# Kernel tuning notes

Measured on AMD Instinct MI355X. Metric: run time of the kernel, lower is better.

## Reference

```python
import jax, jax.numpy as jnp
import numpy as np

UNITS = 512

def _c(r, i):
    return jax.lax.complex(r, i)

# BSSD's elementwise_* activations act on real and imag parts separately (split activation)
def _csig(z):
    return _c(jax.nn.sigmoid(z.real), jax.nn.sigmoid(z.imag))

def _ctanh(z):
    return _c(jnp.tanh(z.real), jnp.tanh(z.imag))

def setup_inputs() -> dict:
    key = jax.random.key(0)
    ks = jax.random.split(key, 6)
    B, T, N, U = 16, 2000, 512, UNITS
    f = lambda k, s, sc: jax.random.normal(k, s, jnp.float32) * sc
    return {
        'x_real': f(ks[0], (B, T, N), 1.0),
        'x_imag': f(ks[1], (B, T, N), 1.0),
        'W_real': f(ks[2], (N, 4 * U), 0.03),
        'W_imag': f(ks[3], (N, 4 * U), 0.03),
        'U_real': f(ks[4], (U, 4 * U), 0.03),
        'U_imag': f(ks[5], (U, 4 * U), 0.03),
        'b_real': jnp.zeros((4 * U,), jnp.float32),
        'b_imag': jnp.zeros((4 * U,), jnp.float32),
    }

def reference(x_real, x_imag, W_real, W_imag, U_real, U_imag, b_real, b_imag):
    Uc = UNITS
    x = _c(x_real, x_imag)                       # [B,T,N] complex64
    W = _c(W_real, W_imag)                       # [N,4U]
    Um = _c(U_real, U_imag)                      # [U,4U]
    b = _c(b_real, b_imag)                       # [4U]
    # input contribution precomputed for all steps (one big GEMM)
    zx = jnp.einsum('bti,ij->btj', x, W) + b     # [B,T,4U]
    zx = jnp.swapaxes(zx, 0, 1)                  # [T,B,4U]
    B = x.shape[0]
    h0 = jnp.zeros((B, Uc), zx.dtype)
    c0 = jnp.zeros((B, Uc), zx.dtype)

    def step(carry, z_t):
        h, c = carry
        z = z_t + h @ Um                         # [B,4U]
        a = _ctanh(z[:, :Uc])
        i = _csig(z[:, Uc:2 * Uc])
        f = _csig(z[:, 2 * Uc:3 * Uc])
        o = _csig(z[:, 3 * Uc:])
        c = a * i + f * c
        h = o * _ctanh(c)                        # activation='tanh'
        return (h, c), h

    _, hs = jax.lax.scan(step, (h0, c0), zx)     # [T,B,U]
    hs = jnp.swapaxes(hs, 0, 1)                  # [B,T,U]
    # return real/imag stacked so output dtype is float32
    return jnp.stack([hs.real, hs.imag], axis=-1)  # [B,T,U,2]
```

## Files before the change

### kernel.cpp

```cpp
#include <hip/hip_runtime.h>
#include <cstdint>
#include <cstddef>

#define B_   16
#define T_   2000
#define NIN  512
#define U_   512
#define G4   2048
#define KP   1024
#define JP   4096
#define M_   32000
#define NGRP 8
#define MPG  32
#define SCAN_BLOCKS (NGRP * MPG)
#define LDSROW 2112

typedef __attribute__((ext_vector_type(8))) short bf16x8;
typedef __attribute__((ext_vector_type(4))) float f32x4;
typedef __attribute__((ext_vector_type(2))) int i32x2;

#define MFMA(a, b, c) __builtin_amdgcn_mfma_f32_16x16x32_bf16((a), (b), (c), 0, 0, 0)

__device__ __forceinline__ unsigned short f2bf(float f) {
  unsigned u = __builtin_bit_cast(unsigned, f);
  u = (u + 0x7FFFu + ((u >> 16) & 1u)) >> 16;
  return (unsigned short)u;
}
__device__ __forceinline__ float bf2f(unsigned short h) {
  unsigned u = ((unsigned)h) << 16;
  return __builtin_bit_cast(float, u);
}
__device__ __forceinline__ float sigm(float x) {
  return 1.0f / (1.0f + __expf(-x));
}
__device__ __forceinline__ float tanh_f(float x) {
  float cx = fminf(fmaxf(x, -15.0f), 15.0f);
  float e = __expf(2.0f * cx);
  return (e - 1.0f) / (e + 1.0f);
}

__device__ __forceinline__ void ld32_l3_sync(const void* p, uint4& a, uint4& b) {
  asm volatile("global_load_dwordx4 %0, %2, off sc0 sc1\n\t"
               "global_load_dwordx4 %1, %3, off sc0 sc1\n\t"
               "s_waitcnt vmcnt(0)"
               : "=&v"(a), "=&v"(b)
               : "v"(p), "v"((const void*)((const char*)p + 16))
               : "memory");
  __builtin_amdgcn_sched_barrier(0);
}
__device__ __forceinline__ void st8_l3(void* p, i32x2 v) {
  asm volatile("global_store_dwordx2 %0, %1, off sc0 sc1" :: "v"(p), "v"(v) : "memory");
}

__global__ __launch_bounds__(256) void k_convert_x(const float* __restrict__ xr,
                                                   const float* __restrict__ xi,
                                                   unsigned short* __restrict__ Ab) {
  int i = blockIdx.x * 256 + threadIdx.x;
  int m = i >> 6;
  int k0 = (i & 63) << 3;
  if (m >= M_) return;
  const float* pr = xr + (size_t)m * NIN + k0;
  const float* pi = xi + (size_t)m * NIN + k0;
  float4 r0 = *reinterpret_cast<const float4*>(pr);
  float4 r1 = *reinterpret_cast<const float4*>(pr + 4);
  float4 i0 = *reinterpret_cast<const float4*>(pi);
  float4 i1 = *reinterpret_cast<const float4*>(pi + 4);
  uint4 v0, v1;
  v0.x = f2bf(r0.x) | ((unsigned)f2bf(i0.x) << 16);
  v0.y = f2bf(r0.y) | ((unsigned)f2bf(i0.y) << 16);
  v0.z = f2bf(r0.z) | ((unsigned)f2bf(i0.z) << 16);
  v0.w = f2bf(r0.w) | ((unsigned)f2bf(i0.w) << 16);
  v1.x = f2bf(r1.x) | ((unsigned)f2bf(i1.x) << 16);
  v1.y = f2bf(r1.y) | ((unsigned)f2bf(i1.y) << 16);
  v1.z = f2bf(r1.z) | ((unsigned)f2bf(i1.z) << 16);
  v1.w = f2bf(r1.w) | ((unsigned)f2bf(i1.w) << 16);
  unsigned short* dst = Ab + (size_t)m * KP + 2 * k0;
  *reinterpret_cast<uint4*>(dst) = v0;
  *reinterpret_cast<uint4*>(dst + 8) = v1;
}

__global__ __launch_bounds__(256) void k_pack_B(const float* __restrict__ Wr,
                                                const float* __restrict__ Wi,
                                                unsigned short* __restrict__ Bt) {
  int i = blockIdx.x * 256 + threadIdx.x;
  if (i >= JP * KP) return;
  int jp = i >> 10;
  int k = i & 1023;
  int p = jp >> 11;
  int j = jp & 2047;
  int u = k >> 1;
  int pl = k & 1;
  float v;
  if (p == 0) {
    v = pl ? -Wi[(size_t)u * G4 + j] : Wr[(size_t)u * G4 + j];
  } else {
    v = pl ? Wr[(size_t)u * G4 + j] : Wi[(size_t)u * G4 + j];
  }
  Bt[i] = f2bf(v);
}

__global__ __launch_bounds__(256) void k_gemm_zx(const unsigned short* __restrict__ A,
                                                 const unsigned short* __restrict__ Bt,
                                                 unsigned short* __restrict__ zx) {
  int bid = blockIdx.x;
  int nt = bid & 31;
  int mt = bid >> 5;
  int tid = threadIdx.x;
  int lane = tid & 63;
  int wid = tid >> 6;
  int wm = wid >> 1, wn = wid & 1;
  int l15 = lane & 15;
  int kb = (lane >> 4) << 3;
  int rowb = mt * 128 + wm * 64;
  int colb = nt * 128 + wn * 64;

  const unsigned short* ap[4];
  const unsigned short* bp[4];
#pragma unroll
  for (int x = 0; x < 4; ++x) {
    ap[x] = A + (size_t)(rowb + x * 16 + l15) * KP + kb;
    bp[x] = Bt + (size_t)(colb + x * 16 + l15) * KP + kb;
  }

  f32x4 acc[4][4];
#pragma unroll
  for (int mi = 0; mi < 4; ++mi)
#pragma unroll
    for (int ni = 0; ni < 4; ++ni) acc[mi][ni] = (f32x4){0.f, 0.f, 0.f, 0.f};

#pragma unroll 2
  for (int k = 0; k < KP; k += 32) {
    bf16x8 av[4], bv[4];
#pragma unroll
    for (int x = 0; x < 4; ++x) {
      av[x] = *reinterpret_cast<const bf16x8*>(ap[x] + k);
      bv[x] = *reinterpret_cast<const bf16x8*>(bp[x] + k);
    }
#pragma unroll
    for (int mi = 0; mi < 4; ++mi)
#pragma unroll
      for (int ni = 0; ni < 4; ++ni)
        acc[mi][ni] = MFMA(av[mi], bv[ni], acc[mi][ni]);
  }

  int rq = (lane >> 4) << 2;
#pragma unroll
  for (int mi = 0; mi < 4; ++mi) {
#pragma unroll
    for (int r = 0; r < 4; ++r) {
      int m = rowb + mi * 16 + rq + r;
      int bbv = m / T_;
      int tv = m - bbv * T_;
      size_t rowoff = (size_t)(tv * 16 + bbv) * (G4 * 2);
#pragma unroll
      for (int ni = 0; ni < 4; ++ni) {
        int jp2 = colb + ni * 16 + l15;
        int p = jp2 >> 11;
        int j = jp2 & 2047;
        zx[rowoff + (size_t)j * 2 + p] = f2bf(acc[mi][ni][r]);
      }
    }
  }
}

__global__ __launch_bounds__(512, 2) void k_scan(
    const unsigned short* __restrict__ zx,
    const unsigned short* __restrict__ Ub,
    const float* __restrict__ brp,
    const float* __restrict__ bip,
    char* __restrict__ hb2,
    float* __restrict__ out) {
  const int bid = blockIdx.x;
  const int tid = threadIdx.x;
  const int lane = tid & 63;
  const int w = tid >> 6;
  const int l15 = lane & 15;
  const int g = bid & 7;
  const int m = bid >> 3;

  __shared__ char lds_h[2 * LDSROW];
  __shared__ float zp[2][132];

  const int p_ = w >> 2, q_ = w & 3;
  const unsigned short* uptr =
      Ub + (size_t)(p_ * 2048 + q_ * 512 + m * 16 + l15) * KP + ((lane >> 4) << 3);
  bf16x8 uf[32];
#pragma unroll
  for (int kk = 0; kk < 32; ++kk)
    uf[kk] = *reinterpret_cast<const bf16x8*>(uptr + kk * 32);
#pragma unroll
  for (int kk = 0; kk < 32; ++kk)
    asm volatile("" : "+v"(uf[kk]));

  const int gb = tid >> 4;
  const int gu = tid & 15;
  const int u = m * 16 + gu;
  const int bglob = g * 2 + gb;
  float brg[4], big[4];
  if (tid < 32) {
#pragma unroll
    for (int q = 0; q < 4; ++q) {
      brg[q] = brp[q * 512 + u];
      big[q] = bip[q * 512 + u];
    }
  }
  float cr = 0.f, ci = 0.f;

  char* hgrp = hb2 + (size_t)g * 16384;

  const int srow = tid >> 7;
  const int sbyte = (tid & 127) * 16;

  const int arow = (l15 & 1) * LDSROW;
  const int achunk = (lane >> 4) * 16;

  unsigned zprev[4];
  if (tid < 32) {
    const unsigned* zt = (const unsigned*)zx + (size_t)bglob * 2048;
#pragma unroll
    for (int q = 0; q < 4; ++q) zprev[q] = zt[q * 512 + u];
  }

  for (int t = 0; t < T_; ++t) {
    const int par = t & 1;

    if (tid < 256) {
      const char* src = hgrp + par * 8192 + tid * 32;
      uint4 v0, v1;
      for (;;) {
        ld32_l3_sync(src, v0, v1);
        if ((int)v0.y >= t && (int)v0.w >= t &&
            (int)v1.y >= t && (int)v1.w >= t) break;
        __builtin_amdgcn_s_sleep(1);
      }
      uint4 hq;
      hq.x = v0.x;
      hq.y = v0.z;
      hq.z = v1.x;
      hq.w = v1.z;
      *reinterpret_cast<uint4*>(lds_h + srow * LDSROW + sbyte) = hq;
    }
    __syncthreads();

    unsigned zloc[4];
    if (tid < 32) {
#pragma unroll
      for (int q = 0; q < 4; ++q) zloc[q] = zprev[q];
      int tp = t + 1 < T_ ? t + 1 : t;
      const unsigned* zt = (const unsigned*)zx + (size_t)(tp * 16 + bglob) * 2048;
#pragma unroll
      for (int q = 0; q < 4; ++q) zprev[q] = zt[q * 512 + u];
    }

    f32x4 a0 = {0.f, 0.f, 0.f, 0.f};
    f32x4 a1 = {0.f, 0.f, 0.f, 0.f};
    f32x4 a2 = {0.f, 0.f, 0.f, 0.f};
    f32x4 a3 = {0.f, 0.f, 0.f, 0.f};
#pragma unroll
    for (int kk = 0; kk < 32; kk += 4) {
      bf16x8 x0 = *reinterpret_cast<const bf16x8*>(lds_h + arow + (kk + 0) * 64 + achunk);
      bf16x8 x1 = *reinterpret_cast<const bf16x8*>(lds_h + arow + (kk + 1) * 64 + achunk);
      bf16x8 x2 = *reinterpret_cast<const bf16x8*>(lds_h + arow + (kk + 2) * 64 + achunk);
      bf16x8 x3 = *reinterpret_cast<const bf16x8*>(lds_h + arow + (kk + 3) * 64 + achunk);
      a0 = MFMA(x0, uf[kk + 0], a0);
      a1 = MFMA(x1, uf[kk + 1], a1);
      a2 = MFMA(x2, uf[kk + 2], a2);
      a3 = MFMA(x3, uf[kk + 3], a3);
    }
    if (lane < 16) {
      f32x4 s = (a0 + a1) + (a2 + a3);
      zp[0][w * 16 + lane] = s[0];
      zp[1][w * 16 + lane] = s[1];
    }
    __syncthreads();

    if (tid < 32) {
      float zr[4], zi[4];
#pragma unroll
      for (int q = 0; q < 4; ++q) {
        zr[q] = zp[gb][q * 16 + gu] + brg[q] +
                bf2f((unsigned short)(zloc[q] & 0xFFFFu));
        zi[q] = zp[gb][64 + q * 16 + gu] + big[q] +
                bf2f((unsigned short)(zloc[q] >> 16));
      }
      float ar = tanh_f(zr[0]), ai = tanh_f(zi[0]);
      float ir = sigm(zr[1]), ii = sigm(zi[1]);
      float fr = sigm(zr[2]), fi = sigm(zi[2]);
      float og_r = sigm(zr[3]), og_i = sigm(zi[3]);
      float ncr = ar * ir - ai * ii + fr * cr - fi * ci;
      float nci = ar * ii + ai * ir + fr * ci + fi * cr;
      cr = ncr;
      ci = nci;
      float tr = tanh_f(cr), ti = tanh_f(ci);
      float hr = og_r * tr - og_i * ti;
      float hi = og_r * ti + og_i * tr;

      i32x2 rec;
      rec.x = (int)((unsigned)f2bf(hr) | ((unsigned)f2bf(hi) << 16));
      rec.y = t + 1;
      st8_l3(hgrp + (par ^ 1) * 8192 + (size_t)(gb * 512 + u) * 8, rec);

      float2 hv;
      hv.x = hr;
      hv.y = hi;
      *reinterpret_cast<float2*>(out + ((size_t)(bglob * T_ + t) * U_ + u) * 2) = hv;
    }
  }
}

extern "C" void kernel_launch(void* const* d_in, const int* in_sizes, int n_in,
                              void* d_out, int out_size, void* d_ws, size_t ws_size,
                              hipStream_t stream) {
  const float* xr = (const float*)d_in[0];
  const float* xi = (const float*)d_in[1];
  const float* Wr = (const float*)d_in[2];
  const float* Wi = (const float*)d_in[3];
  const float* Ur = (const float*)d_in[4];
  const float* Ui = (const float*)d_in[5];
  const float* br = (const float*)d_in[6];
  const float* bi = (const float*)d_in[7];

  const size_t SZ_ZX = (size_t)M_ * G4 * 2 * 2;
  const size_t SZ_AB = (size_t)M_ * KP * 2;
  const size_t SZ_BT = (size_t)JP * KP * 2;
  const size_t SZ_HB2 = (size_t)NGRP * 16384;
  const size_t OFF_ZX = 0;
  const size_t OFF_AB = OFF_ZX + SZ_ZX;
  const size_t OFF_BW = OFF_AB + SZ_AB;
  const size_t OFF_BU = OFF_BW + SZ_BT;
  const size_t OFF_HB = OFF_BU + SZ_BT;
  const size_t NEEDED = OFF_HB + SZ_HB2;
  if (ws_size < NEEDED) return;

  char* ws = (char*)d_ws;
  unsigned short* zx = (unsigned short*)(ws + OFF_ZX);
  unsigned short* Ab = (unsigned short*)(ws + OFF_AB);
  unsigned short* BtW = (unsigned short*)(ws + OFF_BW);
  unsigned short* BtU = (unsigned short*)(ws + OFF_BU);
  char* hb2 = ws + OFF_HB;

  hipMemsetAsync(ws + OFF_HB, 0, SZ_HB2, stream);

  hipLaunchKernelGGL(k_convert_x, dim3(8000), dim3(256), 0, stream, xr, xi, Ab);
  hipLaunchKernelGGL(k_pack_B, dim3(16384), dim3(256), 0, stream, Wr, Wi, BtW);
  hipLaunchKernelGGL(k_pack_B, dim3(16384), dim3(256), 0, stream, Ur, Ui, BtU);
  hipLaunchKernelGGL(k_gemm_zx, dim3(250 * 32), dim3(256), 0, stream, Ab, BtW, zx);
  hipLaunchKernelGGL(k_scan, dim3(SCAN_BLOCKS), dim3(512), 0, stream, zx, BtU,
                     br, bi, hb2, (float*)d_out);
}
```

Baseline: 5.416 ms.

## Split scan into two independent batch streams interleaved per step with shuffle reduction

The recurrent scan now treats the two batch rows of each group as separate streams with their own h buffers and flags. It alternates phases so one stream's MFMA work overlaps the other stream's cross-block wait. The MFMA output layout is remapped so each wave owns two units, which lets a wave shuffle replace the LDS partial-sum buffer and the second __syncthreads. The cost is twice as many global flag polls and barriers per time step, and the launch bound drops to one block per SIMD.

```diff
diff --git a/kernel.cpp b/kernel.cpp
--- a/kernel.cpp
+++ b/kernel.cpp
@@ -13,7 +13,6 @@
 #define NGRP 8
 #define MPG  32
 #define SCAN_BLOCKS (NGRP * MPG)
-#define LDSROW 2112
 
 typedef __attribute__((ext_vector_type(8))) short bf16x8;
 typedef __attribute__((ext_vector_type(4))) float f32x4;
@@ -39,13 +38,10 @@
   return (e - 1.0f) / (e + 1.0f);
 }
 
-__device__ __forceinline__ void ld32_l3_sync(const void* p, uint4& a, uint4& b) {
-  asm volatile("global_load_dwordx4 %0, %2, off sc0 sc1\n\t"
-               "global_load_dwordx4 %1, %3, off sc0 sc1\n\t"
+__device__ __forceinline__ void ld16_l3_sync(const void* p, uint4& a) {
+  asm volatile("global_load_dwordx4 %0, %1, off sc0 sc1\n\t"
                "s_waitcnt vmcnt(0)"
-               : "=&v"(a), "=&v"(b)
-               : "v"(p), "v"((const void*)((const char*)p + 16))
-               : "memory");
+               : "=&v"(a) : "v"(p) : "memory");
   __builtin_amdgcn_sched_barrier(0);
 }
 __device__ __forceinline__ void st8_l3(void* p, i32x2 v) {
@@ -163,7 +159,7 @@
   }
 }
 
-__global__ __launch_bounds__(512, 2) void k_scan(
+__global__ __launch_bounds__(512, 1) void k_scan(
     const unsigned short* __restrict__ zx,
     const unsigned short* __restrict__ Ub,
     const float* __restrict__ brp,
@@ -178,12 +174,13 @@
   const int g = bid & 7;
   const int m = bid >> 3;
 
-  __shared__ char lds_h[2 * LDSROW];
-  __shared__ float zp[2][132];
-
-  const int p_ = w >> 2, q_ = w & 3;
+  __shared__ char lds_h[2][2][2048];
+
+  const int c_ = l15 >> 1, ul_ = l15 & 1;
+  const int p_ = c_ >> 2, q_ = c_ & 3;
   const unsigned short* uptr =
-      Ub + (size_t)(p_ * 2048 + q_ * 512 + m * 16 + l15) * KP + ((lane >> 4) << 3);
+      Ub + (size_t)(p_ * 2048 + q_ * 512 + m * 16 + w * 2 + ul_) * KP +
+      ((lane >> 4) << 3);
   bf16x8 uf[32];
 #pragma unroll
   for (int kk = 0; kk < 32; ++kk)
@@ -192,120 +189,106 @@
   for (int kk = 0; kk < 32; ++kk)
     asm volatile("" : "+v"(uf[kk]));
 
-  const int gb = tid >> 4;
-  const int gu = tid & 15;
-  const int u = m * 16 + gu;
-  const int bglob = g * 2 + gb;
+  const int u = m * 16 + w * 2 + (lane & 1);
   float brg[4], big[4];
-  if (tid < 32) {
+  unsigned zvA[4], zvB[4];
+  if (lane < 2) {
 #pragma unroll
     for (int q = 0; q < 4; ++q) {
       brg[q] = brp[q * 512 + u];
       big[q] = bip[q * 512 + u];
     }
-  }
-  float cr = 0.f, ci = 0.f;
-
-  char* hgrp = hb2 + (size_t)g * 16384;
-
-  const int srow = tid >> 7;
-  const int sbyte = (tid & 127) * 16;
-
-  const int arow = (l15 & 1) * LDSROW;
+    const unsigned* zt0 = (const unsigned*)zx + (size_t)(g * 2 + 0) * 2048;
+    const unsigned* zt1 = (const unsigned*)zx + (size_t)(g * 2 + 1) * 2048;
+#pragma unroll
+    for (int q = 0; q < 4; ++q) {
+      zvA[q] = zt0[q * 512 + u];
+      zvB[q] = zt1[q * 512 + u];
+    }
+  }
+  float crA = 0.f, ciA = 0.f, crB = 0.f, ciB = 0.f;
+
+  char* hgrp = hb2 + (size_t)g * 32768;
   const int achunk = (lane >> 4) * 16;
 
-  unsigned zprev[4];
-  if (tid < 32) {
-    const unsigned* zt = (const unsigned*)zx + (size_t)bglob * 2048;
-#pragma unroll
-    for (int q = 0; q < 4; ++q) zprev[q] = zt[q * 512 + u];
-  }
-
-  for (int t = 0; t < T_; ++t) {
-    const int par = t & 1;
-
-    if (tid < 256) {
-      const char* src = hgrp + par * 8192 + tid * 32;
-      uint4 v0, v1;
-      for (;;) {
-        ld32_l3_sync(src, v0, v1);
-        if ((int)v0.y >= t && (int)v0.w >= t &&
-            (int)v1.y >= t && (int)v1.w >= t) break;
-        __builtin_amdgcn_s_sleep(1);
-      }
-      uint4 hq;
-      hq.x = v0.x;
-      hq.y = v0.z;
-      hq.z = v1.x;
-      hq.w = v1.z;
-      *reinterpret_cast<uint4*>(lds_h + srow * LDSROW + sbyte) = hq;
-    }
-    __syncthreads();
-
-    unsigned zloc[4];
-    if (tid < 32) {
-#pragma unroll
-      for (int q = 0; q < 4; ++q) zloc[q] = zprev[q];
-      int tp = t + 1 < T_ ? t + 1 : t;
-      const unsigned* zt = (const unsigned*)zx + (size_t)(tp * 16 + bglob) * 2048;
-#pragma unroll
-      for (int q = 0; q < 4; ++q) zprev[q] = zt[q * 512 + u];
-    }
-
-    f32x4 a0 = {0.f, 0.f, 0.f, 0.f};
-    f32x4 a1 = {0.f, 0.f, 0.f, 0.f};
-    f32x4 a2 = {0.f, 0.f, 0.f, 0.f};
-    f32x4 a3 = {0.f, 0.f, 0.f, 0.f};
-#pragma unroll
-    for (int kk = 0; kk < 32; kk += 4) {
-      bf16x8 x0 = *reinterpret_cast<const bf16x8*>(lds_h + arow + (kk + 0) * 64 + achunk);
-      bf16x8 x1 = *reinterpret_cast<const bf16x8*>(lds_h + arow + (kk + 1) * 64 + achunk);
-      bf16x8 x2 = *reinterpret_cast<const bf16x8*>(lds_h + arow + (kk + 2) * 64 + achunk);
-      bf16x8 x3 = *reinterpret_cast<const bf16x8*>(lds_h + arow + (kk + 3) * 64 + achunk);
-      a0 = MFMA(x0, uf[kk + 0], a0);
-      a1 = MFMA(x1, uf[kk + 1], a1);
-      a2 = MFMA(x2, uf[kk + 2], a2);
-      a3 = MFMA(x3, uf[kk + 3], a3);
-    }
-    if (lane < 16) {
-      f32x4 s = (a0 + a1) + (a2 + a3);
-      zp[0][w * 16 + lane] = s[0];
-      zp[1][w * 16 + lane] = s[1];
-    }
-    __syncthreads();
-
-    if (tid < 32) {
-      float zr[4], zi[4];
-#pragma unroll
-      for (int q = 0; q < 4; ++q) {
-        zr[q] = zp[gb][q * 16 + gu] + brg[q] +
-                bf2f((unsigned short)(zloc[q] & 0xFFFFu));
-        zi[q] = zp[gb][64 + q * 16 + gu] + big[q] +
-                bf2f((unsigned short)(zloc[q] >> 16));
-      }
-      float ar = tanh_f(zr[0]), ai = tanh_f(zi[0]);
-      float ir = sigm(zr[1]), ii = sigm(zi[1]);
-      float fr = sigm(zr[2]), fi = sigm(zi[2]);
-      float og_r = sigm(zr[3]), og_i = sigm(zi[3]);
-      float ncr = ar * ir - ai * ii + fr * cr - fi * ci;
-      float nci = ar * ii + ai * ir + fr * ci + fi * cr;
-      cr = ncr;
-      ci = nci;
-      float tr = tanh_f(cr), ti = tanh_f(ci);
-      float hr = og_r * tr - og_i * ti;
-      float hi = og_r * ti + og_i * tr;
-
-      i32x2 rec;
-      rec.x = (int)((unsigned)f2bf(hr) | ((unsigned)f2bf(hi) << 16));
-      rec.y = t + 1;
-      st8_l3(hgrp + (par ^ 1) * 8192 + (size_t)(gb * 512 + u) * 8, rec);
-
-      float2 hv;
-      hv.x = hr;
-      hv.y = hi;
-      *reinterpret_cast<float2*>(out + ((size_t)(bglob * T_ + t) * U_ + u) * 2) = hv;
-    }
-  }
+#define PHASE(S, TCUR, PAR, CR, CI, ZV)                                        \
+  {                                                                            \
+    if (tid < 256) {                                                           \
+      const char* psrc = hgrp + (S)*8192 + (PAR)*4096 + tid * 16;              \
+      uint4 pv;                                                                \
+      for (;;) {                                                               \
+        ld16_l3_sync(psrc, pv);                                                \
+        if ((int)pv.y >= (TCUR) && (int)pv.w >= (TCUR)) break;                 \
+        __builtin_amdgcn_s_sleep(1);                                           \
+      }                                                                        \
+      unsigned* ld2 = (unsigned*)(lds_h[S][PAR] + tid * 8);                    \
+      ld2[0] = pv.x;                                                           \
+      ld2[1] = pv.z;                                                           \
+    }                                                                          \
+    __syncthreads();                                                           \
+    f32x4 a0 = {0.f, 0.f, 0.f, 0.f};                                           \
+    f32x4 a1 = {0.f, 0.f, 0.f, 0.f};                                           \
+    f32x4 a2 = {0.f, 0.f, 0.f, 0.f};                                           \
+    f32x4 a3 = {0.f, 0.f, 0.f, 0.f};                                           \
+    _Pragma("unroll")                                                          \
+    for (int kk = 0; kk < 32; kk += 4) {                                       \
+      const char* ab = lds_h[S][PAR] + achunk;                                 \
+      bf16x8 x0 = *(const bf16x8*)(ab + (kk + 0) * 64);                        \
+      bf16x8 x1 = *(const bf16x8*)(ab + (kk + 1) * 64);                        \
+      bf16x8 x2 = *(const bf16x8*)(ab + (kk + 2) * 64);                        \
+      bf16x8 x3 = *(const bf16x8*)(ab + (kk + 3) * 64);                        \
+      a0 = MFMA(x0, uf[kk + 0], a0);                                           \
+      a1 = MFMA(x1, uf[kk + 1], a1);                                           \
+      a2 = MFMA(x2, uf[kk + 2], a2);                                           \
+      a3 = MFMA(x3, uf[kk + 3], a3);                                           \
+    }                                                                          \
+    float zsum = (a0[0] + a1[0]) + (a2[0] + a3[0]);                            \
+    float val[8];                                                              \
+    _Pragma("unroll")                                                          \
+    for (int cc = 0; cc < 8; ++cc)                                             \
+      val[cc] = __shfl(zsum, cc * 2 + (lane & 1));                             \
+    if (lane < 2) {                                                            \
+      float zr[4], zi[4];                                                      \
+      _Pragma("unroll")                                                        \
+      for (int q = 0; q < 4; ++q) {                                            \
+        zr[q] = val[q] + brg[q] + bf2f((unsigned short)((ZV)[q] & 0xFFFFu));   \
+        zi[q] = val[4 + q] + big[q] + bf2f((unsigned short)((ZV)[q] >> 16));   \
+      }                                                                        \
+      float ar = tanh_f(zr[0]), ai = tanh_f(zi[0]);                            \
+      float ir = sigm(zr[1]), ii = sigm(zi[1]);                                \
+      float fr = sigm(zr[2]), fi = sigm(zi[2]);                                \
+      float og_r = sigm(zr[3]), og_i = sigm(zi[3]);                            \
+      float ncr = ar * ir - ai * ii + fr * (CR) - fi * (CI);                   \
+      float nci = ar * ii + ai * ir + fr * (CI) + fi * (CR);                   \
+      (CR) = ncr;                                                              \
+      (CI) = nci;                                                              \
+      float tr = tanh_f(CR), ti = tanh_f(CI);                                  \
+      float hr = og_r * tr - og_i * ti;                                        \
+      float hi = og_r * ti + og_i * tr;                                        \
+      i32x2 rec;                                                               \
+      rec.x = (int)((unsigned)f2bf(hr) | ((unsigned)f2bf(hi) << 16));          \
+      rec.y = (TCUR) + 1;                                                      \
+      st8_l3(hgrp + (S)*8192 + ((PAR) ^ 1) * 4096 + u * 8, rec);               \
+      float2 hv;                                                               \
+      hv.x = hr;                                                               \
+      hv.y = hi;                                                               \
+      *reinterpret_cast<float2*>(                                              \
+          out + ((size_t)((g * 2 + (S)) * T_ + (TCUR)) * U_ + u) * 2) = hv;    \
+      int tp = (TCUR) + 1 < T_ ? (TCUR) + 1 : (TCUR);                          \
+      const unsigned* zt =                                                     \
+          (const unsigned*)zx + (size_t)(tp * 16 + g * 2 + (S)) * 2048;        \
+      _Pragma("unroll")                                                        \
+      for (int q = 0; q < 4; ++q) (ZV)[q] = zt[q * 512 + u];                   \
+    }                                                                          \
+  }
+
+  for (int tt = 0; tt < T_; tt += 2) {
+    PHASE(0, tt, 0, crA, ciA, zvA)
+    PHASE(1, tt, 0, crB, ciB, zvB)
+    PHASE(0, tt + 1, 1, crA, ciA, zvA)
+    PHASE(1, tt + 1, 1, crB, ciB, zvB)
+  }
+#undef PHASE
 }
 
 extern "C" void kernel_launch(void* const* d_in, const int* in_sizes, int n_in,
@@ -323,7 +306,7 @@
   const size_t SZ_ZX = (size_t)M_ * G4 * 2 * 2;
   const size_t SZ_AB = (size_t)M_ * KP * 2;
   const size_t SZ_BT = (size_t)JP * KP * 2;
-  const size_t SZ_HB2 = (size_t)NGRP * 16384;
+  const size_t SZ_HB2 = (size_t)NGRP * 32768;
   const size_t OFF_ZX = 0;
   const size_t OFF_AB = OFF_ZX + SZ_ZX;
   const size_t OFF_BW = OFF_AB + SZ_AB;
```

Measured after the change: 6.981 ms. 28.9% more time.

## Halve scan block to 256 threads, each wave holding two U column tiles

Applied to the files above, without the earlier changes.

The recurrent scan kernel drops from 512 to 256 threads per block. Each wave now keeps two 16-column tiles of the recurrent weight matrix in registers (64 bf16x8 fragments) and reuses each loaded h fragment for two MFMAs, which cuts LDS reads and block-wide barrier cost per timestep. The s_sleep in the spin-wait poll is also removed to lower wake-up latency. The cost is much higher register pressure per thread, a longer serial MFMA chain per wave, and heavier polling traffic on the global flags.

```diff
diff --git a/kernel.cpp b/kernel.cpp
--- a/kernel.cpp
+++ b/kernel.cpp
@@ -163,7 +163,7 @@
   }
 }
 
-__global__ __launch_bounds__(512, 2) void k_scan(
+__global__ __launch_bounds__(256, 1) void k_scan(
     const unsigned short* __restrict__ zx,
     const unsigned short* __restrict__ Ub,
     const float* __restrict__ brp,
@@ -181,16 +181,26 @@
   __shared__ char lds_h[2 * LDSROW];
   __shared__ float zp[2][132];
 
-  const int p_ = w >> 2, q_ = w & 3;
-  const unsigned short* uptr =
-      Ub + (size_t)(p_ * 2048 + q_ * 512 + m * 16 + l15) * KP + ((lane >> 4) << 3);
-  bf16x8 uf[32];
-#pragma unroll
-  for (int kk = 0; kk < 32; ++kk)
-    uf[kk] = *reinterpret_cast<const bf16x8*>(uptr + kk * 32);
-#pragma unroll
-  for (int kk = 0; kk < 32; ++kk)
-    asm volatile("" : "+v"(uf[kk]));
+  bf16x8 uf0[32], uf1[32];
+  {
+    const int c0 = w * 2, c1 = w * 2 + 1;
+    const unsigned short* up0 =
+        Ub + (size_t)((c0 >> 2) * 2048 + (c0 & 3) * 512 + m * 16 + l15) * KP +
+        ((lane >> 4) << 3);
+    const unsigned short* up1 =
+        Ub + (size_t)((c1 >> 2) * 2048 + (c1 & 3) * 512 + m * 16 + l15) * KP +
+        ((lane >> 4) << 3);
+#pragma unroll
+    for (int kk = 0; kk < 32; ++kk) {
+      uf0[kk] = *reinterpret_cast<const bf16x8*>(up0 + kk * 32);
+      uf1[kk] = *reinterpret_cast<const bf16x8*>(up1 + kk * 32);
+    }
+#pragma unroll
+    for (int kk = 0; kk < 32; ++kk) {
+      asm volatile("" : "+v"(uf0[kk]));
+      asm volatile("" : "+v"(uf1[kk]));
+    }
+  }
 
   const int gb = tid >> 4;
   const int gu = tid & 15;
@@ -224,14 +234,13 @@
   for (int t = 0; t < T_; ++t) {
     const int par = t & 1;
 
-    if (tid < 256) {
+    {
       const char* src = hgrp + par * 8192 + tid * 32;
       uint4 v0, v1;
       for (;;) {
         ld32_l3_sync(src, v0, v1);
         if ((int)v0.y >= t && (int)v0.w >= t &&
             (int)v1.y >= t && (int)v1.w >= t) break;
-        __builtin_amdgcn_s_sleep(1);
       }
       uint4 hq;
       hq.x = v0.x;
@@ -257,20 +266,21 @@
     f32x4 a2 = {0.f, 0.f, 0.f, 0.f};
     f32x4 a3 = {0.f, 0.f, 0.f, 0.f};
 #pragma unroll
-    for (int kk = 0; kk < 32; kk += 4) {
+    for (int kk = 0; kk < 32; kk += 2) {
       bf16x8 x0 = *reinterpret_cast<const bf16x8*>(lds_h + arow + (kk + 0) * 64 + achunk);
       bf16x8 x1 = *reinterpret_cast<const bf16x8*>(lds_h + arow + (kk + 1) * 64 + achunk);
-      bf16x8 x2 = *reinterpret_cast<const bf16x8*>(lds_h + arow + (kk + 2) * 64 + achunk);
-      bf16x8 x3 = *reinterpret_cast<const bf16x8*>(lds_h + arow + (kk + 3) * 64 + achunk);
-      a0 = MFMA(x0, uf[kk + 0], a0);
-      a1 = MFMA(x1, uf[kk + 1], a1);
-      a2 = MFMA(x2, uf[kk + 2], a2);
-      a3 = MFMA(x3, uf[kk + 3], a3);
+      a0 = MFMA(x0, uf0[kk + 0], a0);
+      a2 = MFMA(x0, uf1[kk + 0], a2);
+      a1 = MFMA(x1, uf0[kk + 1], a1);
+      a3 = MFMA(x1, uf1[kk + 1], a3);
     }
     if (lane < 16) {
-      f32x4 s = (a0 + a1) + (a2 + a3);
-      zp[0][w * 16 + lane] = s[0];
-      zp[1][w * 16 + lane] = s[1];
+      f32x4 s0 = a0 + a1;
+      f32x4 s1 = a2 + a3;
+      zp[0][(w * 2 + 0) * 16 + lane] = s0[0];
+      zp[1][(w * 2 + 0) * 16 + lane] = s0[1];
+      zp[0][(w * 2 + 1) * 16 + lane] = s1[0];
+      zp[1][(w * 2 + 1) * 16 + lane] = s1[1];
     }
     __syncthreads();
 
@@ -345,6 +355,6 @@
   hipLaunchKernelGGL(k_pack_B, dim3(16384), dim3(256), 0, stream, Wr, Wi, BtW);
   hipLaunchKernelGGL(k_pack_B, dim3(16384), dim3(256), 0, stream, Ur, Ui, BtU);
   hipLaunchKernelGGL(k_gemm_zx, dim3(250 * 32), dim3(256), 0, stream, Ab, BtW, zx);
-  hipLaunchKernelGGL(k_scan, dim3(SCAN_BLOCKS), dim3(512), 0, stream, zx, BtU,
+  hipLaunchKernelGGL(k_scan, dim3(SCAN_BLOCKS), dim3(256), 0, stream, zx, BtU,
                      br, bi, hb2, (float*)d_out);
 }
```

Result: slower. 6.954 ms (+28.4%).

## Stage zx GEMM tiles through swizzled LDS with double-buffered direct global-to-LDS loads

Applied to the files above, without the earlier changes.

The input-projection GEMM used to read A and B fragments straight from global memory into registers. Each wave duplicated those loads, and nothing overlapped them with compute. It now stages 128x64 tiles of A and Bt into double-buffered LDS using global_load_lds, XOR-swizzling columns to avoid bank conflicts, and overlaps the next tile's load with the MFMAs on the current one. This adds LDS traffic and a barrier per k-tile. It only affects the precompute GEMM, while the serial scan likely dominates total time.

```diff
diff --git a/kernel.cpp b/kernel.cpp
--- a/kernel.cpp
+++ b/kernel.cpp
@@ -14,10 +14,14 @@
 #define MPG  32
 #define SCAN_BLOCKS (NGRP * MPG)
 #define LDSROW 2112
+#define BKE  64
 
 typedef __attribute__((ext_vector_type(8))) short bf16x8;
 typedef __attribute__((ext_vector_type(4))) float f32x4;
 typedef __attribute__((ext_vector_type(2))) int i32x2;
+
+typedef __attribute__((address_space(1))) const unsigned AS1U;
+typedef __attribute__((address_space(3))) unsigned AS3U;
 
 #define MFMA(a, b, c) __builtin_amdgcn_mfma_f32_16x16x32_bf16((a), (b), (c), 0, 0, 0)
 
@@ -102,47 +106,88 @@
 __global__ __launch_bounds__(256) void k_gemm_zx(const unsigned short* __restrict__ A,
                                                  const unsigned short* __restrict__ Bt,
                                                  unsigned short* __restrict__ zx) {
+  __shared__ char AbL[2][128 * BKE * 2];
+  __shared__ char BbL[2][128 * BKE * 2];
+
   int bid = blockIdx.x;
   int nt = bid & 31;
   int mt = bid >> 5;
   int tid = threadIdx.x;
   int lane = tid & 63;
-  int wid = tid >> 6;
-  int wm = wid >> 1, wn = wid & 1;
+  int wv = tid >> 6;
+  int wm = wv >> 1, wn = wv & 1;
   int l15 = lane & 15;
-  int kb = (lane >> 4) << 3;
+  int kq = lane >> 4;
+
+  const int srow_l = lane >> 3;
+  const int scol = lane & 7;
+
+#define STAGE(BUF, KT)                                                         \
+  {                                                                            \
+    const int k0_ = (KT)*BKE;                                                  \
+    _Pragma("unroll")                                                          \
+    for (int inst = 0; inst < 4; ++inst) {                                     \
+      int r0_ = wv * 32 + inst * 8;                                            \
+      int ra_ = r0_ + srow_l;                                                  \
+      int ca_ = scol ^ (ra_ & 7);                                              \
+      const unsigned short* ga_ =                                              \
+          A + (size_t)(mt * 128 + ra_) * KP + k0_ + ca_ * 8;                   \
+      __builtin_amdgcn_global_load_lds((AS1U*)ga_,                             \
+                                       (AS3U*)&AbL[BUF][r0_ * 128], 16, 0, 0); \
+      const unsigned short* gb_ =                                              \
+          Bt + (size_t)(nt * 128 + ra_) * KP + k0_ + ca_ * 8;                  \
+      __builtin_amdgcn_global_load_lds((AS1U*)gb_,                             \
+                                       (AS3U*)&BbL[BUF][r0_ * 128], 16, 0, 0); \
+    }                                                                          \
+  }
+
+  f32x4 acc[4][4];
+#pragma unroll
+  for (int mi = 0; mi < 4; ++mi)
+#pragma unroll
+    for (int ni = 0; ni < 4; ++ni) acc[mi][ni] = (f32x4){0.f, 0.f, 0.f, 0.f};
+
+#define COMPUTE(BUF)                                                           \
+  {                                                                            \
+    _Pragma("unroll")                                                          \
+    for (int sl = 0; sl < 2; ++sl) {                                           \
+      bf16x8 av[4], bv[4];                                                     \
+      _Pragma("unroll")                                                        \
+      for (int x = 0; x < 4; ++x) {                                            \
+        int ra_ = wm * 64 + x * 16 + l15;                                      \
+        av[x] = *reinterpret_cast<const bf16x8*>(                              \
+            AbL[BUF] + ra_ * 128 + ((sl * 64 + kq * 16) ^ ((ra_ & 7) << 4)));  \
+        int rb_ = wn * 64 + x * 16 + l15;                                      \
+        bv[x] = *reinterpret_cast<const bf16x8*>(                              \
+            BbL[BUF] + rb_ * 128 + ((sl * 64 + kq * 16) ^ ((rb_ & 7) << 4)));  \
+      }                                                                        \
+      _Pragma("unroll")                                                        \
+      for (int mi = 0; mi < 4; ++mi)                                           \
+        _Pragma("unroll")                                                      \
+        for (int ni = 0; ni < 4; ++ni)                                         \
+          acc[mi][ni] = MFMA(av[mi], bv[ni], acc[mi][ni]);                     \
+    }                                                                          \
+  }
+
+  STAGE(0, 0)
+  asm volatile("s_waitcnt vmcnt(0)" ::: "memory");
+  __syncthreads();
+
+  for (int kt = 0; kt < 16; kt += 2) {
+    STAGE(1, kt + 1)
+    COMPUTE(0)
+    asm volatile("s_waitcnt vmcnt(0)" ::: "memory");
+    __syncthreads();
+    if (kt + 2 < 16) STAGE(0, kt + 2)
+    COMPUTE(1)
+    asm volatile("s_waitcnt vmcnt(0)" ::: "memory");
+    __syncthreads();
+  }
+#undef STAGE
+#undef COMPUTE
+
   int rowb = mt * 128 + wm * 64;
   int colb = nt * 128 + wn * 64;
-
-  const unsigned short* ap[4];
-  const unsigned short* bp[4];
-#pragma unroll
-  for (int x = 0; x < 4; ++x) {
-    ap[x] = A + (size_t)(rowb + x * 16 + l15) * KP + kb;
-    bp[x] = Bt + (size_t)(colb + x * 16 + l15) * KP + kb;
-  }
-
-  f32x4 acc[4][4];
-#pragma unroll
-  for (int mi = 0; mi < 4; ++mi)
-#pragma unroll
-    for (int ni = 0; ni < 4; ++ni) acc[mi][ni] = (f32x4){0.f, 0.f, 0.f, 0.f};
-
-#pragma unroll 2
-  for (int k = 0; k < KP; k += 32) {
-    bf16x8 av[4], bv[4];
-#pragma unroll
-    for (int x = 0; x < 4; ++x) {
-      av[x] = *reinterpret_cast<const bf16x8*>(ap[x] + k);
-      bv[x] = *reinterpret_cast<const bf16x8*>(bp[x] + k);
-    }
-#pragma unroll
-    for (int mi = 0; mi < 4; ++mi)
-#pragma unroll
-      for (int ni = 0; ni < 4; ++ni)
-        acc[mi][ni] = MFMA(av[mi], bv[ni], acc[mi][ni]);
-  }
-
   int rq = (lane >> 4) << 2;
 #pragma unroll
   for (int mi = 0; mi < 4; ++mi) {
```

Result: faster. 4.907 ms (median of 2 runs) (-9.4%).
